# Performance work log

Measured on AMD Instinct MI355X. Metric: run time of the kernel, lower is better.

## Reference

```python
import jax, jax.numpy as jnp
import numpy as np

B, CIN, MID, COUT, H, W = 4, 256, 128, 64, 128, 128
WS, HEADS = 8, 8
HD = MID // HEADS          # head dim = 16
N = WS * WS                # tokens per window = 64


def conv2d(x, w, pad=0, groups=1):
    return jax.lax.conv_general_dilated(
        x, w, (1, 1), ((pad, pad), (pad, pad)),
        feature_group_count=groups,
        dimension_numbers=('NCHW', 'OIHW', 'NCHW'))


def bn(x, g, b):  # eval-mode BatchNorm folded to per-channel affine
    return x * g[None, :, None, None] + b[None, :, None, None]


def setup_inputs() -> dict:
    key = jax.random.key(0)
    ks = jax.random.split(key, 32)
    nrm = lambda i, sh, s: jax.random.normal(ks[i], sh, jnp.float32) * s
    return {
        'x': nrm(0, (B, CIN, H, W), 1.0),
        'conv_w': nrm(1, (MID, CIN, 3, 3), 0.03),
        'bn1_g': 1.0 + nrm(2, (MID,), 0.05), 'bn1_b': nrm(3, (MID,), 0.05),
        'qkv_w': nrm(4, (3 * MID, MID, 1, 1), 0.05),
        'loc1_w': nrm(5, (MID, MID, 3, 3), 0.03),
        'loc1_g': 1.0 + nrm(6, (MID,), 0.05), 'loc1_b': nrm(7, (MID,), 0.05),
        'loc2_w': nrm(8, (MID, MID, 1, 1), 0.05),
        'loc2_g': 1.0 + nrm(9, (MID,), 0.05), 'loc2_b': nrm(10, (MID,), 0.05),
        'rel_table': nrm(11, ((2 * WS - 1) ** 2, HEADS), 0.02),
        'cw_w': nrm(12, (1, 2, 7, 7), 0.1),
        'cw_g': 1.0 + nrm(13, (1,), 0.05), 'cw_b': nrm(14, (1,), 0.05),
        'hc_w': nrm(15, (1, 2, 7, 7), 0.1),
        'hc_g': 1.0 + nrm(16, (1,), 0.05), 'hc_b': nrm(17, (1,), 0.05),
        'hw_w': nrm(18, (1, 2, 7, 7), 0.1),
        'hw_g': 1.0 + nrm(19, (1,), 0.05), 'hw_b': nrm(20, (1,), 0.05),
        'proj_dw': nrm(21, (MID, 1, WS, WS), 0.05),
        'proj_g': 1.0 + nrm(22, (MID,), 0.05), 'proj_b': nrm(23, (MID,), 0.05),
        'proj_pw': nrm(24, (MID, MID, 1, 1), 0.05),
        'up_w': nrm(25, (COUT, MID, 3, 3), 0.03),
    }


def _rel_pos_index():
    coords = np.stack(np.meshgrid(np.arange(WS), np.arange(WS), indexing='ij')).reshape(2, -1)
    rel = (coords[:, :, None] - coords[:, None, :]).transpose(1, 2, 0) + (WS - 1)
    return (rel[:, :, 0] * (2 * WS - 1) + rel[:, :, 1]).reshape(-1)  # [N*N]


def reference(x, conv_w, bn1_g, bn1_b, qkv_w, loc1_w, loc1_g, loc1_b,
              loc2_w, loc2_g, loc2_b, rel_table, cw_w, cw_g, cw_b,
              hc_w, hc_g, hc_b, hw_w, hw_g, hw_b,
              proj_dw, proj_g, proj_b, proj_pw, up_w):
    # DecoderBlock: conv -> BN -> ReLU
    h = jax.nn.relu(bn(conv2d(x, conv_w, pad=1), bn1_g, bn1_b))  # [B,MID,H,W]

    # GlobalLocalAttention
    local = bn(conv2d(h, loc2_w), loc2_g, loc2_b) + bn(conv2d(h, loc1_w, pad=1), loc1_g, loc1_b)

    # windowed qkv (H,W divisible by WS, no pad needed)
    hh, ww = H // WS, W // WS
    qkv = conv2d(h, qkv_w)  # [B, 3*MID, H, W]
    qkv = qkv.reshape(B, 3, HEADS, HD, hh, WS, ww, WS)
    qkv = qkv.transpose(1, 0, 4, 6, 2, 5, 7, 3).reshape(3, B * hh * ww, HEADS, N, HD)
    q, k, v = qkv[0], qkv[1], qkv[2]

    dots = jnp.einsum('bhnd,bhmd->bhnm', q, k) * (HD ** -0.5)  # [Bw,HEADS,N,N]
    bias = rel_table[jnp.asarray(_rel_pos_index())].reshape(N, N, HEADS).transpose(2, 0, 1)
    dots = dots + bias[None]

    # TripletAttention on dots treated as (B', C'=HEADS, H'=N, W'=N)
    def gate(t, w, g, b):
        z = jnp.concatenate([t.max(1, keepdims=True), t.mean(1, keepdims=True)], 1)  # ZPool
        return t * jax.nn.sigmoid(bn(conv2d(z, w, pad=3), g, b))

    d1 = gate(dots.transpose(0, 2, 1, 3), cw_w, cw_g, cw_b).transpose(0, 2, 1, 3)
    d2 = gate(dots.transpose(0, 3, 2, 1), hc_w, hc_g, hc_b).transpose(0, 3, 2, 1)
    d3 = gate(dots, hw_w, hw_g, hw_b)
    dots = (d1 + d2 + d3) / 3.0

    attn = jax.nn.softmax(dots, axis=-1)
    o = jnp.einsum('bhnm,bhmd->bhnd', attn, v)
    o = o.reshape(B, hh, ww, HEADS, WS, WS, HD).transpose(0, 3, 6, 1, 4, 2, 5).reshape(B, MID, H, W)

    # avg+max pooled sigmoid gates (kernel==stride==WS//2, exact reshape pooling)
    kp = WS // 2
    aw = o.reshape(B, MID, H // kp, kp, W)
    Fw = jax.nn.sigmoid(aw.mean(3) + aw.max(3))          # [B,MID,H/4,W]
    ah = o.reshape(B, MID, H, W // kp, kp)
    Fh = jax.nn.sigmoid(ah.mean(4) + ah.max(4))          # [B,MID,H,W/4]
    gmat = jnp.einsum('bchk,bckw->bchw', Fh, Fw)         # [B,MID,H,W]

    out = o * gmat + local
    out = jnp.pad(out, ((0, 0), (0, 0), (0, 1), (0, 1)), mode='reflect')  # pad_out
    # SeparableConvBN proj: depthwise k=WS pad=3 -> BN -> 1x1
    out = conv2d(out, proj_dw, pad=3, groups=MID)
    out = conv2d(bn(out, proj_g, proj_b), proj_pw)
    out = out[:, :, :H, :W]

    # upsample: ConvTranspose2d(k=3, s=2, p=1, op=1) as dilated conv
    up = jax.lax.conv_general_dilated(
        out, up_w, (1, 1), ((1, 2), (1, 2)), lhs_dilation=(2, 2),
        dimension_numbers=('NCHW', 'OIHW', 'NCHW'))  # [B,COUT,2H,2W]
    return up
```

## Files before the change

### kernel.cpp

```cpp
#include <hip/hip_runtime.h>
#include <hip/hip_bf16.h>

typedef __hip_bfloat16 bf16;
typedef __attribute__((ext_vector_type(8))) short short8;
typedef __attribute__((ext_vector_type(4))) float f32x4;

#define DEV __device__ __forceinline__
DEV float b2f(bf16 v){ return __bfloat162float(v); }
DEV bf16 f2b(float v){ return __float2bfloat16(v); }
DEV short f2bs(float v){ union{ bf16 b; short s; } u; u.b = __float2bfloat16(v); return u.s; }
DEV float s2f(short s){ union{ short s; bf16 b; } u; u.s = s; return __bfloat162float(u.b); }
DEV float sigm(float x){ return 1.f/(1.f + expf(-x)); }

#define BB 4
#define CIN 256
#define MID 128
#define COUT 64
#define HH 128
#define WW 128
#define WS 8
#define HEADS 8
#define HD 16
#define NTOK 64
#define NWIN 1024

#define SLOT(row,cq) ((cq) ^ (((row)>>1)&3))

static const size_t OFF_H     = 0;
static const size_t OFF_LOCAL = 33554432;
static const size_t OFF_Q     = 67108864;
static const size_t OFF_K     = 83886080;
static const size_t OFF_V     = 100663296;
static const size_t OFF_DOTS  = 117440512;
static const size_t OFF_Z1    = 184549376;
static const size_t OFF_Z2    = 186646528;
static const size_t OFF_Z3    = 188743680;
static const size_t OFF_G1    = 205520896;
static const size_t OFF_G2    = 207618048;
static const size_t OFF_G3    = 209715200;
static const size_t OFF_HT    = OFF_DOTS + 34078720;

__global__ __launch_bounds__(256) void k_wrep(const float* __restrict__ w, short* __restrict__ w2){
  int i = blockIdx.x*256 + threadIdx.x;
  int ci = i & 255, co = (i >> 8) & 127, kk = i >> 15;
  w2[i] = f2bs(w[(co*256 + ci)*9 + kk]);
}

__global__ void k_xzero(short* __restrict__ xT){
  int t = blockIdx.x*256 + threadIdx.x;
  int ci = t & 255, side = (t >> 8) & 1, row = t >> 9;
  int cpad = side ? 129 : 0;
  xT[((size_t)row*130 + cpad)*256 + ci] = 0;
}

__global__ __launch_bounds__(256) void k_xrep(const float* __restrict__ x, short* __restrict__ xT){
  const int blk = blockIdx.x;
  const int cgrp = blk & 1, cig = (blk >> 1) & 7, r = (blk >> 4) & 127, b = blk >> 11;
  const int c0 = cgrp*64, ci0 = cig*32;
  __shared__ float lds[32][65];
  const int t = threadIdx.x;
  for (int i = t; i < 2048; i += 256){
    int lci = i >> 6, c = i & 63;
    lds[lci][c] = x[((size_t)(b*256 + ci0 + lci)*128 + r)*128 + c0 + c];
  }
  __syncthreads();
  for (int i = t; i < 2048; i += 256){
    int lci = i & 31, cc = i >> 5;
    xT[((size_t)(b*128 + r)*130 + c0 + cc + 1)*256 + ci0 + lci] = f2bs(lds[lci][cc]);
  }
}

__global__ __launch_bounds__(512, 2) void k_conv1m(const short* __restrict__ xT, const short* __restrict__ w2,
      const float* __restrict__ gg, const float* __restrict__ bb, short* __restrict__ hT){
  int blk = blockIdx.x;
  blk = (blk & 7)*32 + (blk >> 3);
  const int cg = blk & 1, y4 = (blk >> 1) & 31, b = blk >> 6;
  const int t = threadIdx.x, lane = t & 63, wave = t >> 6;
  const int quad = lane >> 4, l15 = lane & 15;
  const int row = wave >> 1, xh = wave & 1;
  const int x0w = xh*64;
  __shared__ __align__(16) short smem[31104];
  short* as = smem;
  short* bs = smem + 24960;
  uint4 areg[7], breg[2];
  f32x4 acc[4][4];
  #pragma unroll
  for (int i = 0; i < 4; ++i)
    #pragma unroll
    for (int j = 0; j < 4; ++j) acc[i][j] = (f32x4){0.f,0.f,0.f,0.f};

  auto loadA = [&](int ch){
    const int ci0 = ch*32;
    #pragma unroll
    for (int j = 0; j < 7; ++j){
      int i = t + j*512;
      uint4 val = {0,0,0,0};
      if (j < 6 || i < 3120){
        int sr = i / 520, jj = i - sr*520;
        int col = jj >> 2, cq = jj & 3;
        int g = y4*4 - 1 + sr;
        if ((unsigned)g < 128u)
          val = *(const uint4*)&xT[((size_t)(b*128+g)*130 + col)*256 + ci0 + cq*8];
      }
      areg[j] = val;
    }
  };
  auto writeA = [&](){
    #pragma unroll
    for (int j = 0; j < 7; ++j){
      int i = t + j*512;
      if (j == 6 && i >= 3120) break;
      int sr = i / 520, jj = i - sr*520;
      int col = jj >> 2, cq = jj & 3;
      *(uint4*)&as[((sr*130 + col)*4 + SLOT(col,cq))*8] = areg[j];
    }
  };
  auto loadB = [&](int ch, int ky){
    const int ci0 = ch*32;
    #pragma unroll
    for (int j = 0; j < 2; ++j){
      int i = t + j*512;
      if (j == 1 && t >= 256) break;
      int rr = i >> 2, cq = i & 3;
      int kk = ky*3 + (rr >> 6), co_l = rr & 63;
      breg[j] = *(const uint4*)&w2[((size_t)(kk*128 + cg*64 + co_l))*256 + ci0 + cq*8];
    }
  };
  auto writeB = [&](){
    #pragma unroll
    for (int j = 0; j < 2; ++j){
      int i = t + j*512;
      if (j == 1 && t >= 256) break;
      int rr = i >> 2, cq = i & 3;
      *(uint4*)&bs[(rr*4 + SLOT(rr,cq))*8] = breg[j];
    }
  };
  auto compute = [&](int sr){
    #pragma unroll
    for (int kx = 0; kx < 3; ++kx){
      short8 af[4], bf[4];
      #pragma unroll
      for (int mt = 0; mt < 4; ++mt){
        int col = x0w + mt*16 + l15 + kx;
        af[mt] = *(const short8*)&as[((sr*130 + col)*4 + SLOT(col,quad))*8];
      }
      #pragma unroll
      for (int nt = 0; nt < 4; ++nt){
        int rr = kx*64 + nt*16 + l15;
        bf[nt] = *(const short8*)&bs[(rr*4 + SLOT(rr,quad))*8];
      }
      #pragma unroll
      for (int mt = 0; mt < 4; ++mt)
        #pragma unroll
        for (int nt = 0; nt < 4; ++nt)
          acc[mt][nt] = __builtin_amdgcn_mfma_f32_16x16x32_bf16(af[mt], bf[nt], acc[mt][nt], 0, 0, 0);
    }
  };

  loadA(0); loadB(0, 0);
  #pragma unroll 1
  for (int ch = 0; ch < 8; ++ch){
    __syncthreads();
    writeA(); writeB();
    loadB(ch, 1);
    __syncthreads();
    compute(row + 0);
    __syncthreads();
    writeB(); loadB(ch, 2);
    __syncthreads();
    compute(row + 1);
    __syncthreads();
    writeB();
    if (ch < 7){ loadA(ch+1); loadB(ch+1, 0); }
    __syncthreads();
    compute(row + 2);
  }
  short* tb = smem;
  #pragma unroll 1
  for (int p = 0; p < 2; ++p){
    __syncthreads();
    if ((row >> 1) == p){
      #pragma unroll
      for (int nt = 0; nt < 4; ++nt){
        int cl = nt*16 + l15, co = cg*64 + cl;
        float g = gg[co], bia = bb[co];
        #pragma unroll
        for (int mt = 0; mt < 4; ++mt){
          int xb = x0w + mt*16 + quad*4;
          #pragma unroll
          for (int r2 = 0; r2 < 4; ++r2)
            tb[((row & 1)*128 + xb + r2)*72 + cl] = f2bs(fmaxf(acc[mt][nt][r2]*g + bia, 0.f));
        }
      }
    }
    __syncthreads();
    for (int i = t; i < 2048; i += 512){
      int rr = i >> 10, xx = (i >> 3) & 127, c8 = i & 7;
      *(uint4*)&hT[((size_t)(b*128 + y4*4 + p*2 + rr)*130 + xx + 1)*128 + cg*64 + c8*8] =
        *(const uint4*)&tb[(rr*128 + xx)*72 + c8*8];
    }
  }
}

__global__ void k_hzero(short* __restrict__ hT){
  int t = blockIdx.x*256 + threadIdx.x;
  int ci = t & 127, side = (t >> 7) & 1, row = t >> 8;
  int cpad = side ? 129 : 0;
  hT[((size_t)row*130 + cpad)*128 + ci] = 0;
}

__global__ __launch_bounds__(256) void k_lwrep(const float* __restrict__ w1, const float* __restrict__ g1,
      const float* __restrict__ w2, const float* __restrict__ g2, short* __restrict__ wloc){
  int i = blockIdx.x*256 + threadIdx.x;
  int ci = i & 127, row = (i >> 7) % 384, ky = i / 49152;
  int kx = row >> 7, co = row & 127;
  float v = w1[(co*128 + ci)*9 + ky*3 + kx] * g1[co];
  if (ky == 1 && kx == 1) v += w2[co*128 + ci] * g2[co];
  wloc[i] = f2bs(v);
}

__global__ __launch_bounds__(512, 2) void k_localm(const short* __restrict__ hT, const short* __restrict__ wloc,
      const float* __restrict__ b1, const float* __restrict__ b2, float* __restrict__ out){
  int blk = blockIdx.x;
  blk = (blk & 7)*32 + (blk >> 3);
  const int cg = blk & 1, y4 = (blk >> 1) & 31, b = blk >> 6;
  const int t = threadIdx.x, lane = t & 63, wave = t >> 6;
  const int quad = lane >> 4, l15 = lane & 15;
  const int row = wave >> 1, xh = wave & 1;
  const int x0w = xh*64;
  __shared__ __align__(16) short smem2[31104];
  short* as = smem2;
  short* bs = smem2 + 24960;
  uint4 areg[7], breg[2];
  f32x4 acc[4][4];
  #pragma unroll
  for (int i = 0; i < 4; ++i)
    #pragma unroll
    for (int j = 0; j < 4; ++j) acc[i][j] = (f32x4){0.f,0.f,0.f,0.f};

  auto loadA = [&](int ch){
    const int ci0 = ch*32;
    #pragma unroll
    for (int j = 0; j < 7; ++j){
      int i = t + j*512;
      uint4 val = {0,0,0,0};
      if (j < 6 || i < 3120){
        int sr = i / 520, jj = i - sr*520;
        int col = jj >> 2, cq = jj & 3;
        int g = y4*4 - 1 + sr;
        if ((unsigned)g < 128u)
          val = *(const uint4*)&hT[((size_t)(b*128+g)*130 + col)*128 + ci0 + cq*8];
      }
      areg[j] = val;
    }
  };
  auto writeA = [&](){
    #pragma unroll
    for (int j = 0; j < 7; ++j){
      int i = t + j*512;
      if (j == 6 && i >= 3120) break;
      int sr = i / 520, jj = i - sr*520;
      int col = jj >> 2, cq = jj & 3;
      *(uint4*)&as[((sr*130 + col)*4 + SLOT(col,cq))*8] = areg[j];
    }
  };
  auto loadB = [&](int ch, int ky){
    const int ci0 = ch*32;
    #pragma unroll
    for (int j = 0; j < 2; ++j){
      int i = t + j*512;
      if (j == 1 && t >= 256) break;
      int rr = i >> 2, cq = i & 3;
      int kk = ky*3 + (rr >> 6), co_l = rr & 63;
      breg[j] = *(const uint4*)&wloc[((size_t)(kk*128 + cg*64 + co_l))*128 + ci0 + cq*8];
    }
  };
  auto writeB = [&](){
    #pragma unroll
    for (int j = 0; j < 2; ++j){
      int i = t + j*512;
      if (j == 1 && t >= 256) break;
      int rr = i >> 2, cq = i & 3;
      *(uint4*)&bs[(rr*4 + SLOT(rr,cq))*8] = breg[j];
    }
  };
  auto compute = [&](int sr){
    #pragma unroll
    for (int kx = 0; kx < 3; ++kx){
      short8 af[4], bf[4];
      #pragma unroll
      for (int mt = 0; mt < 4; ++mt){
        int col = x0w + mt*16 + l15 + kx;
        af[mt] = *(const short8*)&as[((sr*130 + col)*4 + SLOT(col,quad))*8];
      }
      #pragma unroll
      for (int nt = 0; nt < 4; ++nt){
        int rr = kx*64 + nt*16 + l15;
        bf[nt] = *(const short8*)&bs[(rr*4 + SLOT(rr,quad))*8];
      }
      #pragma unroll
      for (int mt = 0; mt < 4; ++mt)
        #pragma unroll
        for (int nt = 0; nt < 4; ++nt)
          acc[mt][nt] = __builtin_amdgcn_mfma_f32_16x16x32_bf16(af[mt], bf[nt], acc[mt][nt], 0, 0, 0);
    }
  };

  loadA(0); loadB(0, 0);
  #pragma unroll 1
  for (int ch = 0; ch < 4; ++ch){
    __syncthreads();
    writeA(); writeB();
    loadB(ch, 1);
    __syncthreads();
    compute(row + 0);
    __syncthreads();
    writeB(); loadB(ch, 2);
    __syncthreads();
    compute(row + 1);
    __syncthreads();
    writeB();
    if (ch < 3){ loadA(ch+1); loadB(ch+1, 0); }
    __syncthreads();
    compute(row + 2);
  }
  const int Y = y4*4 + row;
  #pragma unroll
  for (int nt = 0; nt < 4; ++nt){
    int co = cg*64 + nt*16 + l15;
    float bia = b1[co] + b2[co];
    #pragma unroll
    for (int mt = 0; mt < 4; ++mt){
      int xb = x0w + mt*16 + quad*4;
      float4 o4;
      o4.x = acc[mt][nt][0] + bia;
      o4.y = acc[mt][nt][1] + bia;
      o4.z = acc[mt][nt][2] + bia;
      o4.w = acc[mt][nt][3] + bia;
      *(float4*)&out[((size_t)(b*128 + co)*128 + Y)*128 + xb] = o4;
    }
  }
}

__global__ __launch_bounds__(256) void k_wqkvrep(const float* __restrict__ w, short* __restrict__ wqkv){
  int i = blockIdx.x*256 + threadIdx.x;
  wqkv[i] = f2bs(w[i]);
}

__global__ __launch_bounds__(256) void k_qkvm(const short* __restrict__ hT, const short* __restrict__ wqkv,
      bf16* __restrict__ q, bf16* __restrict__ k, bf16* __restrict__ v){
  const int blk = blockIdx.x, ocg = blockIdx.y;
  const int b = blk >> 7, y = blk & 127;
  const int t = threadIdx.x, lane = t & 63, wave = t >> 6;
  const int quad = lane >> 4, l15 = lane & 15;
  const int m0 = (wave >> 1)*64, n0 = (wave & 1)*64;
  __shared__ __align__(16) short asq[4096];
  __shared__ __align__(16) short bsq[4096];
  const short* xrow = hT + ((size_t)(b*128 + y)*130 + 1)*128;
  const short* wk   = wqkv + (size_t)ocg*128*128;
  f32x4 acc[4][4];
  #pragma unroll
  for (int i = 0; i < 4; ++i)
    #pragma unroll
    for (int j = 0; j < 4; ++j) acc[i][j] = (f32x4){0.f,0.f,0.f,0.f};
  for (int ch = 0; ch < 4; ++ch){
    const int ci0 = ch*32;
    __syncthreads();
    for (int i = t; i < 512; i += 256){
      int col = i >> 2, cq = i & 3;
      *(uint4*)&asq[(col*4 + SLOT(col,cq))*8] = *(const uint4*)&xrow[col*128 + ci0 + cq*8];
    }
    for (int i = t; i < 512; i += 256){
      int rr = i >> 2, cq = i & 3;
      *(uint4*)&bsq[(rr*4 + SLOT(rr,cq))*8] = *(const uint4*)&wk[rr*128 + ci0 + cq*8];
    }
    __syncthreads();
    short8 af[4], bf[4];
    #pragma unroll
    for (int mt = 0; mt < 4; ++mt){
      int row = m0 + mt*16 + l15;
      af[mt] = *(const short8*)&asq[(row*4 + SLOT(row,quad))*8];
    }
    #pragma unroll
    for (int nt = 0; nt < 4; ++nt){
      int row = n0 + nt*16 + l15;
      bf[nt] = *(const short8*)&bsq[(row*4 + SLOT(row,quad))*8];
    }
    #pragma unroll
    for (int mt = 0; mt < 4; ++mt)
      #pragma unroll
      for (int nt = 0; nt < 4; ++nt)
        acc[mt][nt] = __builtin_amdgcn_mfma_f32_16x16x32_bf16(af[mt], bf[nt], acc[mt][nt], 0, 0, 0);
  }
  bf16* dst = (ocg == 0) ? q : (ocg == 1) ? k : v;
  const int iy = y & 7, hy = y >> 3;
  #pragma unroll
  for (int nt = 0; nt < 4; ++nt){
    int co = n0 + nt*16 + l15;
    int head = co >> 4, d = co & 15;
    #pragma unroll
    for (int mt = 0; mt < 4; ++mt){
      int xb = m0 + mt*16 + quad*4;
      #pragma unroll
      for (int rr = 0; rr < 4; ++rr){
        int x = xb + rr;
        int bw = b*256 + hy*16 + (x >> 3);
        int n = iy*8 + (x & 7);
        dst[((size_t)(bw*8+head)*64 + n)*16 + d] = f2b(acc[mt][nt][rr]);
      }
    }
  }
}

__global__ __launch_bounds__(256) void k_dots(const bf16* __restrict__ q, const bf16* __restrict__ kk,
      const float* __restrict__ rel, bf16* __restrict__ dots){
  const int bw = blockIdx.x, hd = blockIdx.y;
  __shared__ __align__(16) short qs[64][16];
  __shared__ __align__(16) short ks2[64][16];
  const int t = threadIdx.x;
  const size_t base = (size_t)(bw*8+hd)*1024;
  const short* qp = (const short*)q;
  const short* kp = (const short*)kk;
  if (t < 64){
    *(uint4*)&qs[t][0] = *(const uint4*)&qp[base + t*16];
    *(uint4*)&qs[t][8] = *(const uint4*)&qp[base + t*16 + 8];
  } else if (t < 128){
    int r = t - 64;
    uint4 a0 = *(const uint4*)&kp[base + r*16];
    uint4 a1 = *(const uint4*)&kp[base + r*16 + 8];
    int p = (r >> 4) & 1;
    *(uint4*)&ks2[r][p*8]     = a0;
    *(uint4*)&ks2[r][8 - p*8] = a1;
  }
  __syncthreads();
  const int n = t >> 2, jm = t & 3;
  float qr[16];
  short8 q0 = *(const short8*)&qs[n][0];
  short8 q1 = *(const short8*)&qs[n][8];
  #pragma unroll
  for (int d = 0; d < 8; ++d){ qr[d] = s2f(q0[d]); qr[8+d] = s2f(q1[d]); }
  const int ny = n >> 3, nx = n & 7;
  float a[16];
  #pragma unroll
  for (int mm = 0; mm < 16; ++mm){
    int m = jm*16 + mm;
    int p = (m >> 4) & 1;
    short8 k0 = *(const short8*)&ks2[m][p*8];
    short8 k1 = *(const short8*)&ks2[m][8 - p*8];
    float acc = 0.f;
    #pragma unroll
    for (int d = 0; d < 8; ++d) acc += qr[d]*s2f(k0[d]);
    #pragma unroll
    for (int d = 0; d < 8; ++d) acc += qr[8+d]*s2f(k1[d]);
    int my = m >> 3, mx = m & 7;
    int ridx = (ny - my + 7)*15 + (nx - mx + 7);
    a[mm] = acc*0.25f + rel[ridx*8 + hd];
  }
  short8 s0, s1;
  #pragma unroll
  for (int j = 0; j < 8; ++j){ s0[j] = f2bs(a[j]); s1[j] = f2bs(a[8+j]); }
  short* dp = (short*)dots + base*4 + (size_t)n*64 + jm*16;
  *(short8*)&dp[0] = s0;
  *(short8*)&dp[8] = s1;
}

__global__ __launch_bounds__(256) void k_zall(const bf16* __restrict__ dots,
      bf16* __restrict__ z1, bf16* __restrict__ z2, bf16* __restrict__ z3){
  const int bw = blockIdx.x;
  const int t = threadIdx.x;
  const int q4 = t >> 2, j4 = t & 3;
  __shared__ float sd[64][65];
  float mx3[16], sm3[16];
  #pragma unroll
  for (int i = 0; i < 16; ++i){ mx3[i] = -1e30f; sm3[i] = 0.f; }
  const short* dp = (const short*)dots + (size_t)bw*32768;
  for (int hd = 0; hd < 8; ++hd){
    __syncthreads();
    const short* p = dp + (size_t)hd*4096;
    #pragma unroll
    for (int g = 0; g < 2; ++g){
      short8 s8 = *(const short8*)&p[t*16 + g*8];
      #pragma unroll
      for (int j = 0; j < 8; ++j){
        float vv = s2f(s8[j]);
        sd[q4][j4*16 + g*8 + j] = vv;
        mx3[g*8+j] = fmaxf(mx3[g*8+j], vv);
        sm3[g*8+j] += vv;
      }
    }
    __syncthreads();
    float mx = -1e30f, sm = 0.f;
    #pragma unroll
    for (int m = 0; m < 16; ++m){
      float vv = sd[q4][j4*16 + m];
      mx = fmaxf(mx, vv); sm += vv;
    }
    mx = fmaxf(mx, __shfl_xor(mx, 1, 4));
    mx = fmaxf(mx, __shfl_xor(mx, 2, 4));
    sm += __shfl_xor(sm, 1, 4);
    sm += __shfl_xor(sm, 2, 4);
    if (j4 == 0){
      z2[(size_t)bw*1024 + q4*8 + hd]       = f2b(mx);
      z2[(size_t)bw*1024 + 512 + q4*8 + hd] = f2b(sm*(1.f/64.f));
    }
    float mxc = -1e30f, smc = 0.f;
    #pragma unroll
    for (int nn = 0; nn < 16; ++nn){
      float vv = sd[j4*16 + nn][q4];
      mxc = fmaxf(mxc, vv); smc += vv;
    }
    mxc = fmaxf(mxc, __shfl_xor(mxc, 1, 4));
    mxc = fmaxf(mxc, __shfl_xor(mxc, 2, 4));
    smc += __shfl_xor(smc, 1, 4);
    smc += __shfl_xor(smc, 2, 4);
    if (j4 == 0){
      z1[(size_t)bw*1024 + hd*64 + q4]       = f2b(mxc);
      z1[(size_t)bw*1024 + 512 + hd*64 + q4] = f2b(smc*(1.f/64.f));
    }
  }
  short* zp = (short*)z3 + (size_t)bw*8192;
  short8 o0, o1, p0, p1;
  #pragma unroll
  for (int j = 0; j < 8; ++j){
    o0[j] = f2bs(mx3[j]);        o1[j] = f2bs(mx3[8+j]);
    p0[j] = f2bs(sm3[j]*0.125f); p1[j] = f2bs(sm3[8+j]*0.125f);
  }
  *(short8*)&zp[t*16]          = o0;
  *(short8*)&zp[t*16 + 8]      = o1;
  *(short8*)&zp[4096 + t*16]   = p0;
  *(short8*)&zp[4096 + t*16+8] = p1;
}

__global__ __launch_bounds__(256) void k_gate(const bf16* __restrict__ z, const float* __restrict__ w,
      const float* __restrict__ gg, const float* __restrict__ bb, float* __restrict__ G, int R, int C){
  __shared__ float wsm[98];
  const int t = threadIdx.x;
  if (t < 98) wsm[t] = w[t];
  __syncthreads();
  const int bw = blockIdx.x;
  int p = blockIdx.y*256 + t; if (p >= R*C) return;
  int y = p / C, x = p - y*C;
  float acc = 0.f;
  for (int c = 0; c < 2; ++c)
    for (int ky = 0; ky < 7; ++ky){
      int iy = y + ky - 3; if ((unsigned)iy >= (unsigned)R) continue;
      for (int kx = 0; kx < 7; ++kx){
        int ix = x + kx - 3; if ((unsigned)ix >= (unsigned)C) continue;
        acc += b2f(z[((size_t)(bw*2+c)*R + iy)*C + ix]) * wsm[c*49 + ky*7 + kx];
      }
    }
  G[(size_t)bw*R*C + p] = sigm(acc*gg[0] + bb[0]);
}

__global__ __launch_bounds__(256) void k_gate3(const bf16* __restrict__ z, const float* __restrict__ w,
      const float* __restrict__ gg, const float* __restrict__ bb, float* __restrict__ G){
  const int bw = blockIdx.x;
  __shared__ float pad[2][70][72];
  __shared__ float wsm[98];
  const int t = threadIdx.x;
  if (t < 98) wsm[t] = w[t];
  for (int i = t; i < 2*70*70; i += 256){
    int c = i / 4900, r = i % 4900;
    int py = r / 70, px = r % 70;
    int y = py - 3, x = px - 3;
    float v = 0.f;
    if ((unsigned)y < 64u && (unsigned)x < 64u)
      v = b2f(z[(size_t)bw*8192 + c*4096 + y*64 + x]);
    pad[c][py][px] = v;
  }
  __syncthreads();
  const int tx = t & 15, ty = t >> 4;
  const int x0 = tx*4, y0 = ty*4;
  float acc[4][4] = {};
  #pragma unroll
  for (int c = 0; c < 2; ++c){
    float wr[49];
    #pragma unroll
    for (int kk = 0; kk < 49; ++kk) wr[kk] = wsm[c*49 + kk];
    #pragma unroll
    for (int iy = 0; iy < 10; ++iy){
      float row[10];
      #pragma unroll
      for (int j = 0; j < 10; ++j) row[j] = pad[c][y0+iy][x0+j];
      #pragma unroll
      for (int dy = 0; dy < 4; ++dy){
        const int ky = iy - dy;
        if (ky < 0 || ky > 6) continue;
        #pragma unroll
        for (int kx = 0; kx < 7; ++kx){
          float wv = wr[ky*7 + kx];
          #pragma unroll
          for (int dx = 0; dx < 4; ++dx)
            acc[dy][dx] += wv * row[dx + kx];
        }
      }
    }
  }
  float g0 = gg[0], b0 = bb[0];
  #pragma unroll
  for (int dy = 0; dy < 4; ++dy){
    float4 o4;
    o4.x = sigm(acc[dy][0]*g0 + b0);
    o4.y = sigm(acc[dy][1]*g0 + b0);
    o4.z = sigm(acc[dy][2]*g0 + b0);
    o4.w = sigm(acc[dy][3]*g0 + b0);
    *(float4*)&G[(size_t)bw*4096 + (y0+dy)*64 + x0] = o4;
  }
}

__global__ __launch_bounds__(256) void k_attn(const bf16* __restrict__ dots, const float* __restrict__ G1,
      const float* __restrict__ G2, const float* __restrict__ G3, const bf16* __restrict__ v,
      float* __restrict__ o){
  const int bw = blockIdx.x, hd = blockIdx.y;
  const int b = bw >> 8, wy = (bw >> 4) & 15, wx = bw & 15;
  __shared__ __align__(16) float attn[64][68];
  __shared__ __align__(16) short vst2[16][64];
  __shared__ float invTot[64];
  const int t = threadIdx.x;
  const short* vp = (const short*)v;
  for (int i = t; i < 1024; i += 256){
    int m = i >> 4, d = i & 15;
    int oo = m >> 3, rr = m & 7;
    vst2[d][((oo ^ (d >> 2)) << 3) + rr] = vp[(size_t)(bw*8+hd)*1024 + i];
  }
  const int n = t >> 2, j = t & 3;
  float g2v = G2[(size_t)bw*512 + n*8 + hd];
  const short* dp = (const short*)dots + ((size_t)(bw*8+hd)*64 + n)*64 + j*16;
  const float* g1p = G1 + (size_t)bw*512 + hd*64 + j*16;
  const float* g3p = G3 + (size_t)bw*4096 + n*64 + j*16;
  short8 d0 = *(const short8*)&dp[0];
  short8 d1 = *(const short8*)&dp[8];
  float e[16]; float mx = -1e30f;
  #pragma unroll
  for (int m = 0; m < 16; ++m){
    float dv = s2f(m < 8 ? d0[m] : d1[m-8]) * ((g1p[m] + g2v + g3p[m]) * (1.f/3.f));
    e[m] = dv; mx = fmaxf(mx, dv);
  }
  mx = fmaxf(mx, __shfl_xor(mx, 1, 4));
  mx = fmaxf(mx, __shfl_xor(mx, 2, 4));
  float s = 0.f;
  #pragma unroll
  for (int m = 0; m < 16; ++m){ float ev = expf(e[m]-mx); e[m] = ev; s += ev; }
  s += __shfl_xor(s, 1, 4);
  s += __shfl_xor(s, 2, 4);
  #pragma unroll
  for (int m = 0; m < 16; ++m) attn[n][j*16+m] = e[m];
  if (j == 0) invTot[n] = 1.f/s;
  __syncthreads();
  float acc4[4] = {0.f,0.f,0.f,0.f};
  #pragma unroll
  for (int oo = 0; oo < 8; ++oo){
    float4 a0 = *(const float4*)&attn[n][oo*8];
    float4 a1 = *(const float4*)&attn[n][oo*8+4];
    #pragma unroll
    for (int dd = 0; dd < 4; ++dd){
      short8 v8 = *(const short8*)&vst2[j*4+dd][((oo ^ j) << 3)];
      acc4[dd] += a0.x*s2f(v8[0]) + a0.y*s2f(v8[1]) + a0.z*s2f(v8[2]) + a0.w*s2f(v8[3])
                + a1.x*s2f(v8[4]) + a1.y*s2f(v8[5]) + a1.z*s2f(v8[6]) + a1.w*s2f(v8[7]);
    }
  }
  float it = invTot[n];
  int y = wy*8 + (n>>3), x = wx*8 + (n&7);
  #pragma unroll
  for (int dd = 0; dd < 4; ++dd){
    int c = hd*16 + j*4 + dd;
    o[((size_t)(b*128+c)*128 + y)*128 + x] = acc4[dd]*it;
  }
}

__global__ void k_fw(const float* __restrict__ o, float* __restrict__ Fw){
  int t = blockIdx.x*256 + threadIdx.x; if (t >= 4*128*32*128) return;
  int x = t & 127, kk = (t>>7) & 31, bc = t >> 12;
  const float* p = o + ((size_t)bc*128 + kk*4)*128 + x;
  float mx = -1e30f, sm = 0.f;
  #pragma unroll
  for (int r = 0; r < 4; ++r){ float v = p[r*128]; mx = fmaxf(mx,v); sm += v; }
  Fw[t] = sigm(sm*0.25f + mx);
}
__global__ void k_fh(const float* __restrict__ o, float* __restrict__ Fh){
  int t = blockIdx.x*256 + threadIdx.x; if (t >= 4*128*128*32) return;
  int kk = t & 31, y = (t>>5) & 127, bc = t >> 12;
  const float* p = o + ((size_t)bc*128 + y)*128 + kk*4;
  float mx = -1e30f, sm = 0.f;
  #pragma unroll
  for (int r = 0; r < 4; ++r){ float v = p[r]; mx = fmaxf(mx,v); sm += v; }
  Fh[t] = sigm(sm*0.25f + mx);
}

__global__ __launch_bounds__(256) void k_comb(const float* __restrict__ o, const float* __restrict__ Fh,
      const float* __restrict__ Fw, const float* __restrict__ local, float* __restrict__ comb){
  const int bc = blockIdx.x;
  __shared__ float fh[128][33];
  __shared__ float fw[32][129];
  const int t = threadIdx.x;
  for (int i = t; i < 4096; i += 256) fh[i>>5][i&31]  = Fh[(size_t)bc*4096 + i];
  for (int i = t; i < 4096; i += 256) fw[i>>7][i&127] = Fw[(size_t)bc*4096 + i];
  __syncthreads();
  for (int i = t; i < 16384; i += 256){
    int y = i >> 7, x = i & 127;
    float g = 0.f;
    #pragma unroll
    for (int kk = 0; kk < 32; ++kk) g += fh[y][kk]*fw[kk][x];
    size_t idx = (size_t)bc*16384 + i;
    comb[idx] = o[idx]*g + local[idx];
  }
}

__global__ __launch_bounds__(256) void k_dw(const float* __restrict__ comb, const float* __restrict__ dw,
      const float* __restrict__ gg, const float* __restrict__ bb, float* __restrict__ out){
  const int bz = blockIdx.y;
  const int oy0 = blockIdx.x*16;
  const int c = bz & 127;
  __shared__ float xs[23][136];
  __shared__ float wsm[64];
  const int t = threadIdx.x;
  if (t < 64) wsm[t] = dw[c*64 + t];
  for (int i = t; i < 23*135; i += 256){
    int py = i / 135, px = i - py*135;
    int gy = oy0 + py - 3, gx = px - 3;
    float v = 0.f;
    if (gy >= 0 && gy <= 128 && gx >= 0 && gx <= 128){
      int yy = (gy==128)?126:gy, xx = (gx==128)?126:gx;
      v = comb[((size_t)bz*128 + yy)*128 + xx];
    }
    xs[py][px] = v;
  }
  __syncthreads();
  const int tx = t & 31, ty = t >> 5;
  const int x0 = tx*4, y0 = ty*2;
  float acc[2][4] = {};
  #pragma unroll
  for (int iy = 0; iy < 9; ++iy){
    float row[12];
    *(float4*)&row[0] = *(const float4*)&xs[y0+iy][x0];
    *(float4*)&row[4] = *(const float4*)&xs[y0+iy][x0+4];
    *(float4*)&row[8] = *(const float4*)&xs[y0+iy][x0+8];
    #pragma unroll
    for (int dy = 0; dy < 2; ++dy){
      const int ky = iy - dy;
      if (ky < 0 || ky > 7) continue;
      #pragma unroll
      for (int kx = 0; kx < 8; ++kx){
        float wv = wsm[ky*8 + kx];
        #pragma unroll
        for (int dx = 0; dx < 4; ++dx)
          acc[dy][dx] += wv * row[dx + kx];
      }
    }
  }
  float g = gg[c], bi = bb[c];
  #pragma unroll
  for (int dy = 0; dy < 2; ++dy){
    float4 o4;
    o4.x = acc[dy][0]*g + bi;
    o4.y = acc[dy][1]*g + bi;
    o4.z = acc[dy][2]*g + bi;
    o4.w = acc[dy][3]*g + bi;
    *(float4*)&out[((size_t)bz*128 + oy0 + y0 + dy)*128 + x0] = o4;
  }
}

__global__ void k_omzero(short* __restrict__ omT){
  int t = blockIdx.x*256 + threadIdx.x;
  int ci = t & 127, side = (t >> 7) & 1, row = t >> 8;
  int cpad = side ? 129 : 0;
  omT[((size_t)row*130 + cpad)*128 + ci] = 0;
}

__global__ __launch_bounds__(256) void k_uwrep(const float* __restrict__ w, short* __restrict__ wup){
  int i = blockIdx.x*256 + threadIdx.x;
  int ci = i & 127, co = (i >> 7) & 63, tap = i >> 13;
  wup[i] = f2bs(w[(co*128 + ci)*9 + tap]);
}

__global__ __launch_bounds__(256) void k_pw(const float* __restrict__ p1, const float* __restrict__ w,
      short* __restrict__ omT){
  const int pt = blockIdx.x, cb = blockIdx.y;
  const int P0 = pt*64; const int b = P0 >> 14; const int rem0 = P0 & 16383;
  const int y = rem0 >> 7, x0 = rem0 & 127;
  __shared__ float xsm[128][65];
  __shared__ float wsm[64][129];
  const int tx = threadIdx.x, ty = threadIdx.y, t = ty*16+tx;
  for (int i = t; i < 128*64; i += 256){
    int ci = i >> 6, p = i & 63;
    xsm[ci][p] = p1[(size_t)(b*128+ci)*16384 + rem0 + p];
  }
  for (int i = t; i < 64*128; i += 256){
    int co = i >> 7, ci = i & 127;
    wsm[co][ci] = w[(cb*64+co)*128 + ci];
  }
  __syncthreads();
  float acc[4][4] = {};
  for (int ci = 0; ci < 128; ++ci){
    float hv[4], wv[4];
    #pragma unroll
    for (int jj = 0; jj < 4; ++jj) hv[jj] = xsm[ci][jj*16+tx];
    #pragma unroll
    for (int ii = 0; ii < 4; ++ii) wv[ii] = wsm[ii*16+ty][ci];
    #pragma unroll
    for (int ii = 0; ii < 4; ++ii)
      #pragma unroll
      for (int jj = 0; jj < 4; ++jj) acc[ii][jj] += wv[ii]*hv[jj];
  }
  __syncthreads();
  float* pt_t = &xsm[0][0];
  #pragma unroll
  for (int ii = 0; ii < 4; ++ii)
    #pragma unroll
    for (int jj = 0; jj < 4; ++jj)
      pt_t[(jj*16+tx)*65 + ii*16+ty] = acc[ii][jj];
  __syncthreads();
  for (int i = t; i < 4096; i += 256){
    int px = i >> 6, co_l = i & 63;
    omT[((size_t)(b*128 + y)*130 + x0 + px + 1)*128 + cb*64 + co_l] = f2bs(pt_t[px*65 + co_l]);
  }
}

__global__ __launch_bounds__(256) void k_upm(const short* __restrict__ omT, const short* __restrict__ wup,
      float* __restrict__ out){
  int blk = blockIdx.x;
  blk = (blk & 7)*64 + (blk >> 3);
  const int b = blk >> 7, y = blk & 127;
  const int t = threadIdx.x, lane = t & 63, wave = t >> 6;
  const int quad = lane >> 4, l15 = lane & 15;
  const int m0w = wave*32;
  __shared__ __align__(16) char smem[53504];
  short* asp = (short*)smem;
  short* bsp = (short*)(smem + 16640);
  float* ptile = (float*)smem;
  const int PAR[9] = {3,2,3, 1,0,1, 3,2,3};
  const int ROW[9] = {0,0,0, 0,0,0, 1,1,1};
  const int SHF[9] = {0,0,1, 0,0,1, 0,0,1};
  f32x4 acc[4][2][4];
  #pragma unroll
  for (int p = 0; p < 4; ++p)
    #pragma unroll
    for (int mt = 0; mt < 2; ++mt)
      #pragma unroll
      for (int nt = 0; nt < 4; ++nt) acc[p][mt][nt] = (f32x4){0.f,0.f,0.f,0.f};
  for (int ch = 0; ch < 4; ++ch){
    const int ci0 = ch*32;
    __syncthreads();
    for (int i = t; i < 1040; i += 256){
      int rw = (i >= 520), j = i - rw*520;
      int col = j >> 2, cq = j & 3;
      int row = rw*130 + col;
      uint4 val = {0,0,0,0};
      if (y + rw < 128)
        val = *(const uint4*)&omT[((size_t)(b*128 + y + rw)*130 + col)*128 + ci0 + cq*8];
      *(uint4*)&asp[(row*4 + SLOT(row,cq))*8] = val;
    }
    for (int i = t; i < 2304; i += 256){
      int rr = i >> 2, cq = i & 3;
      *(uint4*)&bsp[(rr*4 + SLOT(rr,cq))*8] = *(const uint4*)&wup[rr*128 + ci0 + cq*8];
    }
    __syncthreads();
    #pragma unroll
    for (int k = 0; k < 9; ++k){
      const int pr = PAR[k], rw = ROW[k], sh = SHF[k];
      if (rw && y == 127) continue;
      short8 af[2], bf[4];
      #pragma unroll
      for (int mt = 0; mt < 2; ++mt){
        int row = rw*130 + m0w + mt*16 + l15 + 1 + sh;
        af[mt] = *(const short8*)&asp[(row*4 + SLOT(row,quad))*8];
      }
      #pragma unroll
      for (int nt = 0; nt < 4; ++nt){
        int row = k*64 + nt*16 + l15;
        bf[nt] = *(const short8*)&bsp[(row*4 + SLOT(row,quad))*8];
      }
      #pragma unroll
      for (int mt = 0; mt < 2; ++mt)
        #pragma unroll
        for (int nt = 0; nt < 4; ++nt)
          acc[pr][mt][nt] = __builtin_amdgcn_mfma_f32_16x16x32_bf16(af[mt], bf[nt], acc[pr][mt][nt], 0, 0, 0);
    }
  }
  #pragma unroll
  for (int p = 0; p < 4; ++p){
    __syncthreads();
    #pragma unroll
    for (int mt = 0; mt < 2; ++mt)
      #pragma unroll
      for (int nt = 0; nt < 4; ++nt){
        int co = nt*16 + l15;
        int xb = m0w + mt*16 + quad*4;
        #pragma unroll
        for (int r = 0; r < 4; ++r)
          ptile[co*132 + xb + r] = acc[p][mt][nt][r];
      }
    __syncthreads();
    int py = p >> 1, px = p & 1;
    int Y = 2*y + py;
    for (int i = t; i < 8192; i += 256){
      int co = i >> 7, xx = i & 127;
      out[((size_t)(b*64 + co)*256 + Y)*256 + 2*xx + px] = ptile[co*132 + xx];
    }
  }
}

extern "C" void kernel_launch(void* const* d_in, const int* in_sizes, int n_in,
                              void* d_out, int out_size, void* d_ws, size_t ws_size,
                              hipStream_t stream) {
  const float* x       = (const float*)d_in[0];
  const float* conv_w  = (const float*)d_in[1];
  const float* bn1_g   = (const float*)d_in[2];
  const float* bn1_b   = (const float*)d_in[3];
  const float* qkv_w   = (const float*)d_in[4];
  const float* loc1_w  = (const float*)d_in[5];
  const float* loc1_g  = (const float*)d_in[6];
  const float* loc1_b  = (const float*)d_in[7];
  const float* loc2_w  = (const float*)d_in[8];
  const float* loc2_g  = (const float*)d_in[9];
  const float* loc2_b  = (const float*)d_in[10];
  const float* rel_t   = (const float*)d_in[11];
  const float* cw_w    = (const float*)d_in[12];
  const float* cw_g    = (const float*)d_in[13];
  const float* cw_b    = (const float*)d_in[14];
  const float* hc_w    = (const float*)d_in[15];
  const float* hc_g    = (const float*)d_in[16];
  const float* hc_b    = (const float*)d_in[17];
  const float* hw_w    = (const float*)d_in[18];
  const float* hw_g    = (const float*)d_in[19];
  const float* hw_b    = (const float*)d_in[20];
  const float* proj_dw = (const float*)d_in[21];
  const float* proj_g  = (const float*)d_in[22];
  const float* proj_b  = (const float*)d_in[23];
  const float* proj_pw = (const float*)d_in[24];
  const float* up_w    = (const float*)d_in[25];

  char* ws = (char*)d_ws;
  float* local  = (float*)(ws + OFF_LOCAL);
  bf16*  q      = (bf16*)(ws + OFF_Q);
  bf16*  k      = (bf16*)(ws + OFF_K);
  bf16*  v      = (bf16*)(ws + OFF_V);
  bf16*  dots   = (bf16*)(ws + OFF_DOTS);
  bf16*  z1     = (bf16*)(ws + OFF_Z1);
  bf16*  z2     = (bf16*)(ws + OFF_Z2);
  bf16*  z3     = (bf16*)(ws + OFF_Z3);
  float* G1     = (float*)(ws + OFF_G1);
  float* G2     = (float*)(ws + OFF_G2);
  float* G3     = (float*)(ws + OFF_G3);
  short* xT     = (short*)(ws + OFF_DOTS);
  short* hT     = (short*)(ws + OFF_HT);
  short* w2bf   = (short*)(ws + OFF_Z1);
  short* wloc   = (short*)(ws + OFF_Z2);
  short* wqkv   = (short*)(ws + OFF_Z3);
  short* omT    = (short*)(ws + OFF_DOTS);
  short* wup    = (short*)(ws + OFF_Z1);
  float* o_img  = (float*)(ws + OFF_Q);
  float* Fh     = (float*)(ws + OFF_DOTS);
  float* Fw     = (float*)(ws + OFF_DOTS + 8388608);
  float* comb   = (float*)(ws + OFF_H);
  float* proj1  = (float*)(ws + OFF_LOCAL);
  float* outp   = (float*)d_out;

  dim3 blk2(16,16);
  k_wrep <<<1152, 256, 0, stream>>>(conv_w, w2bf);
  k_xzero<<<1024, 256, 0, stream>>>(xT);
  k_xrep <<<8192, 256, 0, stream>>>(x, xT);
  k_hzero<<<512, 256, 0, stream>>>(hT);
  k_conv1m<<<256, 512, 0, stream>>>(xT, w2bf, bn1_g, bn1_b, hT);
  k_lwrep<<<576, 256, 0, stream>>>(loc1_w, loc1_g, loc2_w, loc2_g, wloc);
  k_localm<<<256, 512, 0, stream>>>(hT, wloc, loc1_b, loc2_b, local);
  k_wqkvrep<<<192, 256, 0, stream>>>(qkv_w, wqkv);
  k_qkvm <<<dim3(512,3), 256, 0, stream>>>(hT, wqkv, q, k, v);
  k_dots <<<dim3(NWIN,8), 256, 0, stream>>>(q, k, rel_t, dots);
  k_zall <<<NWIN, 256, 0, stream>>>(dots, z1, z2, z3);
  k_gate <<<dim3(NWIN,2),  256, 0, stream>>>(z1, cw_w, cw_g, cw_b, G1, 8, 64);
  k_gate <<<dim3(NWIN,2),  256, 0, stream>>>(z2, hc_w, hc_g, hc_b, G2, 64, 8);
  k_gate3<<<NWIN, 256, 0, stream>>>(z3, hw_w, hw_g, hw_b, G3);
  k_attn <<<dim3(NWIN,8), 256, 0, stream>>>(dots, G1, G2, G3, v, o_img);
  k_fw   <<<8192, 256, 0, stream>>>(o_img, Fw);
  k_fh   <<<8192, 256, 0, stream>>>(o_img, Fh);
  k_comb <<<512, 256, 0, stream>>>(o_img, Fh, Fw, local, comb);
  k_dw   <<<dim3(8, BB*128), 256, 0, stream>>>(comb, proj_dw, proj_g, proj_b, proj1);
  k_omzero<<<512, 256, 0, stream>>>(omT);
  k_uwrep<<<288, 256, 0, stream>>>(up_w, wup);
  k_pw   <<<dim3(1024,2), blk2, 0, stream>>>(proj1, proj_pw, omT);
  k_upm  <<<512, 256, 0, stream>>>(omT, wup, outp);
}
```

Baseline: 665.0 us.

## Split 3x3 conv GEMM kernels into 2-row tiles with 256-thread blocks

```diff
diff --git a/kernel.cpp b/kernel.cpp
--- a/kernel.cpp
+++ b/kernel.cpp
@@ -70,19 +70,18 @@
   }
 }
 
-__global__ __launch_bounds__(512, 2) void k_conv1m(const short* __restrict__ xT, const short* __restrict__ w2,
+__global__ __launch_bounds__(256) void k_conv1m(const short* __restrict__ xT, const short* __restrict__ w2,
       const float* __restrict__ gg, const float* __restrict__ bb, short* __restrict__ hT){
   int blk = blockIdx.x;
-  blk = (blk & 7)*32 + (blk >> 3);
-  const int cg = blk & 1, y4 = (blk >> 1) & 31, b = blk >> 6;
+  blk = (blk & 7)*64 + (blk >> 3);
+  const int cg = blk & 1, y2 = (blk >> 1) & 63, b = blk >> 7;
   const int t = threadIdx.x, lane = t & 63, wave = t >> 6;
   const int quad = lane >> 4, l15 = lane & 15;
-  const int row = wave >> 1, xh = wave & 1;
-  const int x0w = xh*64;
-  __shared__ __align__(16) short smem[31104];
+  const int r = wave >> 1, x0w = (wave & 1)*64;
+  __shared__ __align__(16) short smem[22784];
   short* as = smem;
-  short* bs = smem + 24960;
-  uint4 areg[7], breg[2];
+  short* bs = smem + 16640;
+  uint4 areg[9], breg[3];
   f32x4 acc[4][4];
   #pragma unroll
   for (int i = 0; i < 4; ++i)
@@ -92,13 +91,13 @@
   auto loadA = [&](int ch){
     const int ci0 = ch*32;
     #pragma unroll
-    for (int j = 0; j < 7; ++j){
-      int i = t + j*512;
+    for (int j = 0; j < 9; ++j){
+      int i = t + j*256;
       uint4 val = {0,0,0,0};
-      if (j < 6 || i < 3120){
+      if (i < 2080){
         int sr = i / 520, jj = i - sr*520;
         int col = jj >> 2, cq = jj & 3;
-        int g = y4*4 - 1 + sr;
+        int g = 2*y2 - 1 + sr;
         if ((unsigned)g < 128u)
           val = *(const uint4*)&xT[((size_t)(b*128+g)*130 + col)*256 + ci0 + cq*8];
       }
@@ -107,20 +106,20 @@
   };
   auto writeA = [&](){
     #pragma unroll
-    for (int j = 0; j < 7; ++j){
-      int i = t + j*512;
-      if (j == 6 && i >= 3120) break;
-      int sr = i / 520, jj = i - sr*520;
-      int col = jj >> 2, cq = jj & 3;
-      *(uint4*)&as[((sr*130 + col)*4 + SLOT(col,cq))*8] = areg[j];
+    for (int j = 0; j < 9; ++j){
+      int i = t + j*256;
+      if (i < 2080){
+        int sr = i / 520, jj = i - sr*520;
+        int col = jj >> 2, cq = jj & 3;
+        *(uint4*)&as[((sr*130 + col)*4 + SLOT(col,cq))*8] = areg[j];
+      }
     }
   };
   auto loadB = [&](int ch, int ky){
     const int ci0 = ch*32;
     #pragma unroll
-    for (int j = 0; j < 2; ++j){
-      int i = t + j*512;
-      if (j == 1 && t >= 256) break;
+    for (int j = 0; j < 3; ++j){
+      int i = t + j*256;
       int rr = i >> 2, cq = i & 3;
       int kk = ky*3 + (rr >> 6), co_l = rr & 63;
       breg[j] = *(const uint4*)&w2[((size_t)(kk*128 + cg*64 + co_l))*256 + ci0 + cq*8];
@@ -128,9 +127,8 @@
   };
   auto writeB = [&](){
     #pragma unroll
-    for (int j = 0; j < 2; ++j){
-      int i = t + j*512;
-      if (j == 1 && t >= 256) break;
+    for (int j = 0; j < 3; ++j){
+      int i = t + j*256;
       int rr = i >> 2, cq = i & 3;
       *(uint4*)&bs[(rr*4 + SLOT(rr,cq))*8] = breg[j];
     }
@@ -160,45 +158,36 @@
   loadA(0); loadB(0, 0);
   #pragma unroll 1
   for (int ch = 0; ch < 8; ++ch){
-    __syncthreads();
-    writeA(); writeB();
-    loadB(ch, 1);
-    __syncthreads();
-    compute(row + 0);
-    __syncthreads();
-    writeB(); loadB(ch, 2);
-    __syncthreads();
-    compute(row + 1);
-    __syncthreads();
-    writeB();
-    if (ch < 7){ loadA(ch+1); loadB(ch+1, 0); }
-    __syncthreads();
-    compute(row + 2);
-  }
+    #pragma unroll 1
+    for (int ky = 0; ky < 3; ++ky){
+      __syncthreads();
+      if (ky == 0) writeA();
+      writeB();
+      if (ky < 2) loadB(ch, ky+1);
+      else if (ch < 7){ loadA(ch+1); loadB(ch+1, 0); }
+      __syncthreads();
+      compute(r + ky);
+    }
+  }
+  __syncthreads();
   short* tb = smem;
-  #pragma unroll 1
-  for (int p = 0; p < 2; ++p){
-    __syncthreads();
-    if ((row >> 1) == p){
-      #pragma unroll
-      for (int nt = 0; nt < 4; ++nt){
-        int cl = nt*16 + l15, co = cg*64 + cl;
-        float g = gg[co], bia = bb[co];
-        #pragma unroll
-        for (int mt = 0; mt < 4; ++mt){
-          int xb = x0w + mt*16 + quad*4;
-          #pragma unroll
-          for (int r2 = 0; r2 < 4; ++r2)
-            tb[((row & 1)*128 + xb + r2)*72 + cl] = f2bs(fmaxf(acc[mt][nt][r2]*g + bia, 0.f));
-        }
-      }
-    }
-    __syncthreads();
-    for (int i = t; i < 2048; i += 512){
-      int rr = i >> 10, xx = (i >> 3) & 127, c8 = i & 7;
-      *(uint4*)&hT[((size_t)(b*128 + y4*4 + p*2 + rr)*130 + xx + 1)*128 + cg*64 + c8*8] =
-        *(const uint4*)&tb[(rr*128 + xx)*72 + c8*8];
-    }
+  #pragma unroll
+  for (int nt = 0; nt < 4; ++nt){
+    int cl = nt*16 + l15, co = cg*64 + cl;
+    float g = gg[co], bia = bb[co];
+    #pragma unroll
+    for (int mt = 0; mt < 4; ++mt){
+      int xb = x0w + mt*16 + quad*4;
+      #pragma unroll
+      for (int r2 = 0; r2 < 4; ++r2)
+        tb[(r*128 + xb + r2)*72 + cl] = f2bs(fmaxf(acc[mt][nt][r2]*g + bia, 0.f));
+    }
+  }
+  __syncthreads();
+  for (int i = t; i < 2048; i += 256){
+    int rr = i >> 10, xx = (i >> 3) & 127, c8 = i & 7;
+    *(uint4*)&hT[((size_t)(b*128 + 2*y2 + rr)*130 + xx + 1)*128 + cg*64 + c8*8] =
+      *(const uint4*)&tb[(rr*128 + xx)*72 + c8*8];
   }
 }
 
@@ -219,19 +208,18 @@
   wloc[i] = f2bs(v);
 }
 
-__global__ __launch_bounds__(512, 2) void k_localm(const short* __restrict__ hT, const short* __restrict__ wloc,
+__global__ __launch_bounds__(256) void k_localm(const short* __restrict__ hT, const short* __restrict__ wloc,
       const float* __restrict__ b1, const float* __restrict__ b2, float* __restrict__ out){
   int blk = blockIdx.x;
-  blk = (blk & 7)*32 + (blk >> 3);
-  const int cg = blk & 1, y4 = (blk >> 1) & 31, b = blk >> 6;
+  blk = (blk & 7)*64 + (blk >> 3);
+  const int cg = blk & 1, y2 = (blk >> 1) & 63, b = blk >> 7;
   const int t = threadIdx.x, lane = t & 63, wave = t >> 6;
   const int quad = lane >> 4, l15 = lane & 15;
-  const int row = wave >> 1, xh = wave & 1;
-  const int x0w = xh*64;
-  __shared__ __align__(16) short smem2[31104];
+  const int r = wave >> 1, x0w = (wave & 1)*64;
+  __shared__ __align__(16) short smem2[22784];
   short* as = smem2;
-  short* bs = smem2 + 24960;
-  uint4 areg[7], breg[2];
+  short* bs = smem2 + 16640;
+  uint4 areg[9], breg[3];
   f32x4 acc[4][4];
   #pragma unroll
   for (int i = 0; i < 4; ++i)
@@ -241,13 +229,13 @@
   auto loadA = [&](int ch){
     const int ci0 = ch*32;
     #pragma unroll
-    for (int j = 0; j < 7; ++j){
-      int i = t + j*512;
+    for (int j = 0; j < 9; ++j){
+      int i = t + j*256;
       uint4 val = {0,0,0,0};
-      if (j < 6 || i < 3120){
+      if (i < 2080){
         int sr = i / 520, jj = i - sr*520;
         int col = jj >> 2, cq = jj & 3;
-        int g = y4*4 - 1 + sr;
+        int g = 2*y2 - 1 + sr;
         if ((unsigned)g < 128u)
           val = *(const uint4*)&hT[((size_t)(b*128+g)*130 + col)*128 + ci0 + cq*8];
       }
@@ -256,20 +244,20 @@
   };
   auto writeA = [&](){
     #pragma unroll
-    for (int j = 0; j < 7; ++j){
-      int i = t + j*512;
-      if (j == 6 && i >= 3120) break;
-      int sr = i / 520, jj = i - sr*520;
-      int col = jj >> 2, cq = jj & 3;
-      *(uint4*)&as[((sr*130 + col)*4 + SLOT(col,cq))*8] = areg[j];
+    for (int j = 0; j < 9; ++j){
+      int i = t + j*256;
+      if (i < 2080){
+        int sr = i / 520, jj = i - sr*520;
+        int col = jj >> 2, cq = jj & 3;
+        *(uint4*)&as[((sr*130 + col)*4 + SLOT(col,cq))*8] = areg[j];
+      }
     }
   };
   auto loadB = [&](int ch, int ky){
     const int ci0 = ch*32;
     #pragma unroll
-    for (int j = 0; j < 2; ++j){
-      int i = t + j*512;
-      if (j == 1 && t >= 256) break;
+    for (int j = 0; j < 3; ++j){
+      int i = t + j*256;
       int rr = i >> 2, cq = i & 3;
       int kk = ky*3 + (rr >> 6), co_l = rr & 63;
       breg[j] = *(const uint4*)&wloc[((size_t)(kk*128 + cg*64 + co_l))*128 + ci0 + cq*8];
@@ -277,9 +265,8 @@
   };
   auto writeB = [&](){
     #pragma unroll
-    for (int j = 0; j < 2; ++j){
-      int i = t + j*512;
-      if (j == 1 && t >= 256) break;
+    for (int j = 0; j < 3; ++j){
+      int i = t + j*256;
       int rr = i >> 2, cq = i & 3;
       *(uint4*)&bs[(rr*4 + SLOT(rr,cq))*8] = breg[j];
     }
@@ -309,22 +296,18 @@
   loadA(0); loadB(0, 0);
   #pragma unroll 1
   for (int ch = 0; ch < 4; ++ch){
-    __syncthreads();
-    writeA(); writeB();
-    loadB(ch, 1);
-    __syncthreads();
-    compute(row + 0);
-    __syncthreads();
-    writeB(); loadB(ch, 2);
-    __syncthreads();
-    compute(row + 1);
-    __syncthreads();
-    writeB();
-    if (ch < 3){ loadA(ch+1); loadB(ch+1, 0); }
-    __syncthreads();
-    compute(row + 2);
-  }
-  const int Y = y4*4 + row;
+    #pragma unroll 1
+    for (int ky = 0; ky < 3; ++ky){
+      __syncthreads();
+      if (ky == 0) writeA();
+      writeB();
+      if (ky < 2) loadB(ch, ky+1);
+      else if (ch < 3){ loadA(ch+1); loadB(ch+1, 0); }
+      __syncthreads();
+      compute(r + ky);
+    }
+  }
+  const int Y = 2*y2 + r;
   #pragma unroll
   for (int nt = 0; nt < 4; ++nt){
     int co = cg*64 + nt*16 + l15;
@@ -961,9 +944,9 @@
   k_xzero<<<1024, 256, 0, stream>>>(xT);
   k_xrep <<<8192, 256, 0, stream>>>(x, xT);
   k_hzero<<<512, 256, 0, stream>>>(hT);
-  k_conv1m<<<256, 512, 0, stream>>>(xT, w2bf, bn1_g, bn1_b, hT);
+  k_conv1m<<<512, 256, 0, stream>>>(xT, w2bf, bn1_g, bn1_b, hT);
   k_lwrep<<<576, 256, 0, stream>>>(loc1_w, loc1_g, loc2_w, loc2_g, wloc);
-  k_localm<<<256, 512, 0, stream>>>(hT, wloc, loc1_b, loc2_b, local);
+  k_localm<<<512, 256, 0, stream>>>(hT, wloc, loc1_b, loc2_b, local);
   k_wqkvrep<<<192, 256, 0, stream>>>(qkv_w, wqkv);
   k_qkvm <<<dim3(512,3), 256, 0, stream>>>(hT, wqkv, q, k, v);
   k_dots <<<dim3(NWIN,8), 256, 0, stream>>>(q, k, rel_t, dots);
```

After: 693.4 us. 1.04x slower.
